# Performance work log

Hardware: AMD Instinct MI355X
Metric: run time of the kernel (lower is better)

Reference implementation:

```python
import jax, jax.numpy as jnp
import numpy as np

N_STATE = 1024
N_HEAD = 16
HEAD_DIM = N_STATE // N_HEAD
SEQLENS = [1024, 896, 768, 640, 512, 384, 896, 1024]  # sum = 6144
TOTAL = sum(SEQLENS)


def setup_inputs() -> dict:
    key = jax.random.key(0)
    ks = jax.random.split(key, 8)
    s = 0.02
    cu = jnp.asarray(np.concatenate([[0], np.cumsum(SEQLENS)]), dtype=jnp.int32)
    return {
        "x": jax.random.normal(ks[0], (TOTAL, N_STATE), jnp.float32),
        "cu_seqlens": cu,
        "Wq": jax.random.normal(ks[1], (N_STATE, N_STATE), jnp.float32) * s,
        "bq": jax.random.normal(ks[2], (N_STATE,), jnp.float32) * s,
        "Wk": jax.random.normal(ks[3], (N_STATE, N_STATE), jnp.float32) * s,
        "Wv": jax.random.normal(ks[4], (N_STATE, N_STATE), jnp.float32) * s,
        "bv": jax.random.normal(ks[5], (N_STATE,), jnp.float32) * s,
        "Wo": jax.random.normal(ks[6], (N_STATE, N_STATE), jnp.float32) * s,
        "bo": jax.random.normal(ks[7], (N_STATE,), jnp.float32) * s,
    }


def reference(x, cu_seqlens, Wq, bq, Wk, Wv, bv, Wo, bo):
    # cu_seqlens is a static (host) quantity in the original (used via .tolist())
    cu = np.asarray(jax.device_get(cu_seqlens))
    seqlens = cu[1:] - cu[:-1]
    B = len(seqlens)
    Lmax = int(seqlens.max())

    q = x @ Wq.T + bq              # [T, n_state]
    k = x @ Wk.T                   # key has no bias
    v = x @ Wv.T + bv

    # static pad/unpad index maps (honoring the ragged structure)
    ar = np.arange(Lmax)
    valid = ar[None, :] < seqlens[:, None]             # [B, Lmax]
    idx = np.where(valid, cu[:-1, None] + ar[None, :], 0)
    unpad_idx = np.nonzero(valid.reshape(-1))[0]       # flat positions of real tokens
    valid_j = jnp.asarray(valid)

    def pad(t):  # [T, n_state] -> [B, Lmax, H, D], zeros in padding
        p = jnp.where(valid_j[:, :, None], t[idx], 0.0)
        return p.reshape(B, Lmax, N_HEAD, HEAD_DIM)

    qp, kp, vp = pad(q), pad(k), pad(v)
    scale = HEAD_DIM ** -0.5
    # torch adds the bool mask (True->1.0) after masked_fill(mask==0, -max):
    # valid keys get +1.0 (softmax-invariant shift), invalid keys get -finfo.max
    big_neg = jnp.finfo(x.dtype).max
    add_mask = jnp.where(valid_j, 1.0, -big_neg)[:, None, None, :]  # [B,1,1,Lmax]

    scores = jnp.einsum("bqhd,bkhd->bhqk", qp, kp) * scale + add_mask
    weights = jax.nn.softmax(scores, axis=-1)
    ctx = jnp.einsum("bhqk,bkhd->bqhd", weights, vp)   # [B, Lmax, H, D]
    ctx_flat = ctx.reshape(B * Lmax, N_STATE)[unpad_idx]  # [T, n_state]
    return ctx_flat @ Wo.T + bo
```

## Files before the change

kernel.cpp:

```cpp
#include <hip/hip_runtime.h>

typedef unsigned short u16;
typedef unsigned int u32;
typedef __attribute__((ext_vector_type(8))) short bf16x8;
typedef __attribute__((ext_vector_type(4))) float f32x4;

#define MFMA_BF16(a, b, c) __builtin_amdgcn_mfma_f32_16x16x32_bf16((a), (b), (c), 0, 0, 0)

#define QSCALE 0.18033688011112042f

__device__ __forceinline__ u16 f2bf(float f) {
    union { float f; unsigned u; } v; v.f = f;
    return (u16)((v.u + 0x7FFFu + ((v.u >> 16) & 1u)) >> 16);
}

__device__ __forceinline__ u32 pkbf(float a, float b) {
    union { float f; unsigned u; } x, y; x.f = a; y.f = b;
    return ((x.u + 0x8000u) >> 16) | ((y.u + 0x8000u) & 0xFFFF0000u);
}

__device__ __forceinline__ void async16(const void* g, void* l) {
    __builtin_amdgcn_global_load_lds(
        (const __attribute__((address_space(1))) void*)g,
        (__attribute__((address_space(3))) void*)l, 16, 0, 0);
}

__global__ __launch_bounds__(256) void cvt_all(
    const float* __restrict__ x, const float* __restrict__ Wq, const float* __restrict__ Wk,
    const float* __restrict__ Wv, const float* __restrict__ Wo,
    u16* __restrict__ xb, u16* __restrict__ Wqb, u16* __restrict__ Wkb,
    u16* __restrict__ Wvb, u16* __restrict__ Wob) {
    int b = blockIdx.x;
    const float* src; u16* dst; int base;
    if (b < 6144)      { src = x;  dst = xb;  base = b; }
    else if (b < 7168) { src = Wq; dst = Wqb; base = b - 6144; }
    else if (b < 8192) { src = Wk; dst = Wkb; base = b - 7168; }
    else if (b < 9216) { src = Wv; dst = Wvb; base = b - 8192; }
    else               { src = Wo; dst = Wob; base = b - 9216; }
    int i = base * 256 + threadIdx.x;
    float4 v = ((const float4*)src)[i];
    unsigned long long pk = (unsigned long long)f2bf(v.x)
                          | ((unsigned long long)f2bf(v.y) << 16)
                          | ((unsigned long long)f2bf(v.z) << 32)
                          | ((unsigned long long)f2bf(v.w) << 48);
    *(unsigned long long*)(dst + (size_t)i * 4) = pk;
}

__global__ __launch_bounds__(256) void gemm_qkv(
    const u16* __restrict__ xb,
    const u16* __restrict__ Wqb, const u16* __restrict__ Wkb, const u16* __restrict__ Wvb,
    const float* __restrict__ bq, const float* __restrict__ bv,
    u16* __restrict__ qb, u16* __restrict__ kb, u16* __restrict__ vbT) {
    __shared__ __align__(16) u16 As[2][128 * 64];
    __shared__ __align__(16) u16 Bs[2][128 * 64];
    const int tid = threadIdx.x;

    const int fid = blockIdx.x;
    const int xcd = fid & 7;
    const int slot = fid >> 3;
    const int mloc = slot % 6;
    const int nidx = slot / 6;
    const int m0 = (xcd * 6 + mloc) << 7;
    const int buf = nidx >> 3;
    const int n0 = (nidx & 7) << 7;
    const u16* __restrict__ W = (buf == 0) ? Wqb : (buf == 1) ? Wkb : Wvb;

    const int rr = tid >> 3;
    const int cg = tid & 7;
    const int wv = tid >> 6, lane = tid & 63, g = lane >> 4, c = lane & 15;
    const int wm = (wv & 1) << 6, wn = (wv >> 1) << 6;

    const int sw = (cg ^ (rr & 7)) << 3;
    const u16* gA[4]; const u16* gB[4];
#pragma unroll
    for (int r = 0; r < 4; ++r) {
        gA[r] = xb + (size_t)(m0 + (r << 5) + rr) * 1024 + sw;
        gB[r] = W + (size_t)(n0 + (r << 5) + rr) * 1024 + sw;
    }

    f32x4 zero = {0.f, 0.f, 0.f, 0.f};
    f32x4 acc[4][4];
#pragma unroll
    for (int i = 0; i < 4; ++i)
#pragma unroll
        for (int j = 0; j < 4; ++j) acc[i][j] = zero;

#pragma unroll
    for (int r = 0; r < 4; ++r) {
        async16(gA[r], &As[0][(r << 11) + tid * 8]);
        async16(gB[r], &Bs[0][(r << 11) + tid * 8]);
    }
#pragma unroll
    for (int r = 0; r < 4; ++r) {
        async16(gA[r] + 64, &As[1][(r << 11) + tid * 8]);
        async16(gB[r] + 64, &Bs[1][(r << 11) + tid * 8]);
    }
    asm volatile("s_waitcnt vmcnt(8)" ::: "memory");
    __builtin_amdgcn_s_barrier();
    __builtin_amdgcn_sched_barrier(0);

    for (int kt = 0; kt < 16; ++kt) {
        const int cur = kt & 1;
#pragma unroll
        for (int ks = 0; ks < 2; ++ks) {
            bf16x8 af[4], bb[4];
#pragma unroll
            for (int i = 0; i < 4; ++i) {
                int ra = wm + (i << 4) + c;
                af[i] = *(const bf16x8*)(&As[cur][ra * 64 + ((((ks << 2) + g) ^ (ra & 7)) << 3)]);
                int rb = wn + (i << 4) + c;
                bb[i] = *(const bf16x8*)(&Bs[cur][rb * 64 + ((((ks << 2) + g) ^ (rb & 7)) << 3)]);
            }
#pragma unroll
            for (int i = 0; i < 4; ++i)
#pragma unroll
                for (int j = 0; j < 4; ++j) acc[i][j] = MFMA_BF16(af[i], bb[j], acc[i][j]);
        }
        if (kt == 15) break;
        __builtin_amdgcn_sched_barrier(0);
        __builtin_amdgcn_s_barrier();
        if (kt < 14) {
            const int k0 = (kt + 2) << 6;
#pragma unroll
            for (int r = 0; r < 4; ++r) {
                async16(gA[r] + k0, &As[cur][(r << 11) + tid * 8]);
                async16(gB[r] + k0, &Bs[cur][(r << 11) + tid * 8]);
            }
            asm volatile("s_waitcnt vmcnt(8)" ::: "memory");
        } else {
            asm volatile("s_waitcnt vmcnt(0)" ::: "memory");
        }
        __builtin_amdgcn_s_barrier();
        __builtin_amdgcn_sched_barrier(0);
    }

    if (buf == 0) {
#pragma unroll
        for (int j = 0; j < 4; ++j) {
            int col = n0 + wn + (j << 4) + c;
            float bias = bq[col];
#pragma unroll
            for (int i = 0; i < 4; ++i) {
                int rowb = m0 + wm + (i << 4) + (g << 2);
#pragma unroll
                for (int r = 0; r < 4; ++r)
                    qb[(size_t)(rowb + r) * 1024 + col] = f2bf((acc[i][j][r] + bias) * QSCALE);
            }
        }
    } else if (buf == 1) {
#pragma unroll
        for (int j = 0; j < 4; ++j) {
            int col = n0 + wn + (j << 4) + c;
#pragma unroll
            for (int i = 0; i < 4; ++i) {
                int rowb = m0 + wm + (i << 4) + (g << 2);
#pragma unroll
                for (int r = 0; r < 4; ++r)
                    kb[(size_t)(rowb + r) * 1024 + col] = f2bf(acc[i][j][r]);
            }
        }
    } else {
#pragma unroll
        for (int j = 0; j < 4; ++j) {
            int col = n0 + wn + (j << 4) + c;
            float bias = bv[col];
#pragma unroll
            for (int i = 0; i < 4; ++i) {
                int trow = m0 + wm + (i << 4) + (g << 2);
                unsigned long long pk =
                      (unsigned long long)f2bf(acc[i][j][0] + bias)
                    | ((unsigned long long)f2bf(acc[i][j][1] + bias) << 16)
                    | ((unsigned long long)f2bf(acc[i][j][2] + bias) << 32)
                    | ((unsigned long long)f2bf(acc[i][j][3] + bias) << 48);
                *(unsigned long long*)(vbT + (size_t)col * 6144 + trow) = pk;
            }
        }
    }
}

__global__ __launch_bounds__(256) void gemm_out(
    const u16* __restrict__ ctxb, const u16* __restrict__ Wob,
    const float* __restrict__ bo, float* __restrict__ out) {
    __shared__ __align__(16) u16 As[2][64 * 64];
    __shared__ __align__(16) u16 Bs[2][64 * 64];
    const int tid = threadIdx.x;

    const int fid = blockIdx.x;
    const int xcd = fid & 7;
    const int slot = fid >> 3;
    const int mloc = slot % 12;
    const int nidx = slot / 12;
    const int m0 = (xcd * 12 + mloc) << 6;
    const int n0 = nidx << 6;

    const int rr = tid >> 3, cg = tid & 7;
    const int wv = tid >> 6, lane = tid & 63, g = lane >> 4, c = lane & 15;
    const int wm = (wv & 1) << 5, wn = (wv >> 1) << 5;

    const int sw = (cg ^ (rr & 7)) << 3;
    const u16* gA[2]; const u16* gB[2];
#pragma unroll
    for (int r = 0; r < 2; ++r) {
        gA[r] = ctxb + (size_t)(m0 + (r << 5) + rr) * 1024 + sw;
        gB[r] = Wob + (size_t)(n0 + (r << 5) + rr) * 1024 + sw;
    }

    f32x4 zero = {0.f, 0.f, 0.f, 0.f};
    f32x4 acc[2][2];
#pragma unroll
    for (int i = 0; i < 2; ++i)
#pragma unroll
        for (int j = 0; j < 2; ++j) acc[i][j] = zero;

#pragma unroll
    for (int r = 0; r < 2; ++r) {
        async16(gA[r], &As[0][(r << 11) + tid * 8]);
        async16(gB[r], &Bs[0][(r << 11) + tid * 8]);
    }
#pragma unroll
    for (int r = 0; r < 2; ++r) {
        async16(gA[r] + 64, &As[1][(r << 11) + tid * 8]);
        async16(gB[r] + 64, &Bs[1][(r << 11) + tid * 8]);
    }
    asm volatile("s_waitcnt vmcnt(4)" ::: "memory");
    __builtin_amdgcn_s_barrier();
    __builtin_amdgcn_sched_barrier(0);

    for (int kt = 0; kt < 16; ++kt) {
        const int cur = kt & 1;
#pragma unroll
        for (int ks = 0; ks < 2; ++ks) {
            bf16x8 af[2], bb[2];
#pragma unroll
            for (int i = 0; i < 2; ++i) {
                int ra = wm + (i << 4) + c;
                af[i] = *(const bf16x8*)(&As[cur][ra * 64 + ((((ks << 2) + g) ^ (ra & 7)) << 3)]);
                int rb = wn + (i << 4) + c;
                bb[i] = *(const bf16x8*)(&Bs[cur][rb * 64 + ((((ks << 2) + g) ^ (rb & 7)) << 3)]);
            }
#pragma unroll
            for (int i = 0; i < 2; ++i)
#pragma unroll
                for (int j = 0; j < 2; ++j) acc[i][j] = MFMA_BF16(af[i], bb[j], acc[i][j]);
        }
        if (kt == 15) break;
        __builtin_amdgcn_sched_barrier(0);
        __builtin_amdgcn_s_barrier();
        if (kt < 14) {
            const int k0 = (kt + 2) << 6;
#pragma unroll
            for (int r = 0; r < 2; ++r) {
                async16(gA[r] + k0, &As[cur][(r << 11) + tid * 8]);
                async16(gB[r] + k0, &Bs[cur][(r << 11) + tid * 8]);
            }
            asm volatile("s_waitcnt vmcnt(4)" ::: "memory");
        } else {
            asm volatile("s_waitcnt vmcnt(0)" ::: "memory");
        }
        __builtin_amdgcn_s_barrier();
        __builtin_amdgcn_sched_barrier(0);
    }

#pragma unroll
    for (int j = 0; j < 2; ++j) {
        int col = n0 + wn + (j << 4) + c;
        float bias = bo[col];
#pragma unroll
        for (int i = 0; i < 2; ++i) {
            int rowb = m0 + wm + (i << 4) + (g << 2);
#pragma unroll
            for (int r = 0; r < 4; ++r)
                out[(size_t)(rowb + r) * 1024 + col] = acc[i][j][r] + bias;
        }
    }
}

__global__ __launch_bounds__(256) void attn_kernel(const u16* __restrict__ qb,
                                                   const u16* __restrict__ kb,
                                                   const u16* __restrict__ vbT,
                                                   u16* __restrict__ ctxb) {
    __shared__ __align__(16) u16 Ks[128 * 64];
    __shared__ __align__(16) u16 Vs[64 * 128];
    __shared__ __align__(16) u16 Ps[4 * 2048];

    const int tid = threadIdx.x;
    const int fid = blockIdx.x;
    const int xcd = fid & 7;
    const int slot = fid >> 3;
    const int h = (xcd << 1) + (slot >= 96 ? 1 : 0);
    const int q0 = (slot % 96) << 6;

    const int cuv[9] = {0, 1024, 1920, 2688, 3328, 3840, 4224, 5120, 6144};
    int s0 = 0, e0 = 6144;
#pragma unroll
    for (int i = 1; i < 8; ++i) {
        if (q0 >= cuv[i]) s0 = cuv[i];
        if (q0 < cuv[i] && cuv[i] < e0) e0 = cuv[i];
    }
    const int ntiles = (e0 - s0) >> 7;

    const int wv = tid >> 6, lane = tid & 63, g = lane >> 4, c = lane & 15;
    const int wrow = wv << 4;

    {
        const int rr = tid >> 3, cg = tid & 7;
#pragma unroll
        for (int r = 0; r < 2; ++r) {
            int row = (r << 5) + rr;
            async16(qb + (size_t)(q0 + row) * 1024 + (h << 6) + ((cg ^ (row & 7)) << 3),
                    Ps + (r << 11) + tid * 8);
        }
    }
    __syncthreads();

    bf16x8 qf[2];
#pragma unroll
    for (int ks = 0; ks < 2; ++ks) {
        int row = wrow + c;
        qf[ks] = *(const bf16x8*)(Ps + row * 64 + ((((ks << 2) + g) ^ (row & 7)) << 3));
    }

    float m_run = -1e30f, l_run = 0.f;
    f32x4 zero = {0.f, 0.f, 0.f, 0.f};
    f32x4 oacc[4];
#pragma unroll
    for (int nt = 0; nt < 4; ++nt) oacc[nt] = zero;

    const int pbase = (wv << 11) + c * 128;
    const int c7 = c & 7;

    for (int kt = 0; kt < ntiles; ++kt) {
        const int kv0 = s0 + (kt << 7);
        __syncthreads();
        {
            const int rr = tid >> 3, cg = tid & 7;
#pragma unroll
            for (int r = 0; r < 4; ++r) {
                int row = (r << 5) + rr;
                async16(kb + (size_t)(kv0 + row) * 1024 + (h << 6) + ((cg ^ (row & 7)) << 3),
                        Ks + (r << 11) + tid * 8);
            }
            const int rr2 = tid >> 4, cg2 = tid & 15;
#pragma unroll
            for (int r = 0; r < 4; ++r) {
                int row = (r << 4) + rr2;
                async16(vbT + (size_t)((h << 6) + row) * 6144 + kv0 + ((cg2 ^ (row & 15)) << 3),
                        Vs + (r << 11) + tid * 8);
            }
        }
        __syncthreads();

        f32x4 st[8];
#pragma unroll
        for (int mt = 0; mt < 8; ++mt) st[mt] = zero;
#pragma unroll
        for (int mt = 0; mt < 8; ++mt) {
            int row = (mt << 4) + c;
            int sw = row & 7;
#pragma unroll
            for (int ks = 0; ks < 2; ++ks) {
                bf16x8 kf = *(const bf16x8*)(&Ks[row * 64 + ((((ks << 2) + g) ^ sw) << 3)]);
                st[mt] = MFMA_BF16(kf, qf[ks], st[mt]);
            }
        }

        float mx = st[0][0];
#pragma unroll
        for (int mt = 0; mt < 8; ++mt)
#pragma unroll
            for (int r = 0; r < 4; ++r) mx = fmaxf(mx, st[mt][r]);
        mx = fmaxf(mx, __shfl_xor(mx, 16, 64));
        mx = fmaxf(mx, __shfl_xor(mx, 32, 64));
        float mnew = fmaxf(m_run, mx);
        float alpha = exp2f(m_run - mnew);
        m_run = mnew;

        float rsum = 0.f;
#pragma unroll
        for (int mt = 0; mt < 8; ++mt) {
            float p0 = exp2f(st[mt][0] - mnew);
            float p1 = exp2f(st[mt][1] - mnew);
            float p2 = exp2f(st[mt][2] - mnew);
            float p3 = exp2f(st[mt][3] - mnew);
            rsum += (p0 + p1) + (p2 + p3);
            int ph = ((mt << 2) + g) ^ (c7 << 1);
            *(uint2*)(Ps + pbase + (ph << 2)) = make_uint2(pkbf(p0, p1), pkbf(p2, p3));
        }
        rsum += __shfl_xor(rsum, 16, 64);
        rsum += __shfl_xor(rsum, 32, 64);
        l_run = l_run * alpha + rsum;

        float al[4];
#pragma unroll
        for (int r = 0; r < 4; ++r) al[r] = __shfl(alpha, (g << 2) + r, 16);
#pragma unroll
        for (int nt = 0; nt < 4; ++nt)
#pragma unroll
            for (int r = 0; r < 4; ++r) oacc[nt][r] *= al[r];

#pragma unroll
        for (int ks = 0; ks < 4; ++ks) {
            int pg = ((ks << 2) + g) ^ c7;
            bf16x8 pf = *(const bf16x8*)(Ps + pbase + (pg << 3));
#pragma unroll
            for (int nt = 0; nt < 4; ++nt) {
                int vrow = (nt << 4) + c;
                bf16x8 vf = *(const bf16x8*)(&Vs[vrow * 128 + ((((ks << 2) + g) ^ (vrow & 15)) << 3)]);
                oacc[nt] = MFMA_BF16(pf, vf, oacc[nt]);
            }
        }
    }

    float inv = 1.0f / l_run;
    float invr[4];
#pragma unroll
    for (int r = 0; r < 4; ++r) invr[r] = __shfl(inv, (g << 2) + r, 16);
#pragma unroll
    for (int r = 0; r < 4; ++r) {
        size_t rowoff = (size_t)(q0 + wrow + (g << 2) + r) * 1024 + (h << 6);
#pragma unroll
        for (int nt = 0; nt < 4; ++nt)
            ctxb[rowoff + (nt << 4) + c] = f2bf(oacc[nt][r] * invr[r]);
    }
}

extern "C" void kernel_launch(void* const* d_in, const int* in_sizes, int n_in,
                              void* d_out, int out_size, void* d_ws, size_t ws_size,
                              hipStream_t stream) {
    const float* x  = (const float*)d_in[0];
    const float* Wq = (const float*)d_in[2];
    const float* bq = (const float*)d_in[3];
    const float* Wk = (const float*)d_in[4];
    const float* Wv = (const float*)d_in[5];
    const float* bv = (const float*)d_in[6];
    const float* Wo = (const float*)d_in[7];
    const float* bo = (const float*)d_in[8];
    float* out = (float*)d_out;

    u16* ws = (u16*)d_ws;
    u16* xb   = ws;
    u16* Wqb  = xb + 6291456;
    u16* Wkb  = Wqb + 1048576;
    u16* Wvb  = Wkb + 1048576;
    u16* Wob  = Wvb + 1048576;
    u16* qb   = Wob + 1048576;
    u16* kb   = qb + 6291456;
    u16* vbT  = kb + 6291456;
    u16* ctxb = xb;

    cvt_all<<<10240, 256, 0, stream>>>(x, Wq, Wk, Wv, Wo, xb, Wqb, Wkb, Wvb, Wob);
    gemm_qkv<<<1152, 256, 0, stream>>>(xb, Wqb, Wkb, Wvb, bq, bv, qb, kb, vbT);
    attn_kernel<<<1536, 256, 0, stream>>>(qb, kb, vbT, ctxb);
    gemm_out<<<1536, 256, 0, stream>>>(ctxb, Wob, bo, out);
}
```

Measured before the change: 228.5 us.

## Load attention K/V/Q fragments directly from global memory and skip rescales

The attention kernel drops the shared-memory staging of Q, K and V tiles and the two block barriers per KV tile. Each wave now reads its MFMA operand fragments straight from global memory, relying on L2/cache reuse across the four waves, and launch bounds request 4 blocks per SM for occupancy. Online-softmax rescaling is skipped unless the new row max exceeds the running max by more than 8 in the log2 domain, which removes exp and multiply work on most tiles. In exchange, global loads are redundant across waves and less coalesced. Skipping the rescale lets probabilities reach up to 2^8 before the bf16 packing, which is a small numerical risk.

After: 332.5 us. 1.45x slower.

```diff
diff --git a/kernel.cpp b/kernel.cpp
--- a/kernel.cpp
+++ b/kernel.cpp
@@ -275,12 +275,10 @@
     }
 }
 
-__global__ __launch_bounds__(256) void attn_kernel(const u16* __restrict__ qb,
-                                                   const u16* __restrict__ kb,
-                                                   const u16* __restrict__ vbT,
-                                                   u16* __restrict__ ctxb) {
-    __shared__ __align__(16) u16 Ks[128 * 64];
-    __shared__ __align__(16) u16 Vs[64 * 128];
+__global__ __launch_bounds__(256, 4) void attn_kernel(const u16* __restrict__ qb,
+                                                      const u16* __restrict__ kb,
+                                                      const u16* __restrict__ vbT,
+                                                      u16* __restrict__ ctxb) {
     __shared__ __align__(16) u16 Ps[4 * 2048];
 
     const int tid = threadIdx.x;
@@ -302,23 +300,10 @@
     const int wv = tid >> 6, lane = tid & 63, g = lane >> 4, c = lane & 15;
     const int wrow = wv << 4;
 
-    {
-        const int rr = tid >> 3, cg = tid & 7;
-#pragma unroll
-        for (int r = 0; r < 2; ++r) {
-            int row = (r << 5) + rr;
-            async16(qb + (size_t)(q0 + row) * 1024 + (h << 6) + ((cg ^ (row & 7)) << 3),
-                    Ps + (r << 11) + tid * 8);
-        }
-    }
-    __syncthreads();
-
+    const u16* qp = qb + (size_t)(q0 + wrow + c) * 1024 + (h << 6) + (g << 3);
     bf16x8 qf[2];
-#pragma unroll
-    for (int ks = 0; ks < 2; ++ks) {
-        int row = wrow + c;
-        qf[ks] = *(const bf16x8*)(Ps + row * 64 + ((((ks << 2) + g) ^ (row & 7)) << 3));
-    }
+    qf[0] = *(const bf16x8*)(qp);
+    qf[1] = *(const bf16x8*)(qp + 32);
 
     float m_run = -1e30f, l_run = 0.f;
     f32x4 zero = {0.f, 0.f, 0.f, 0.f};
@@ -329,39 +314,23 @@
     const int pbase = (wv << 11) + c * 128;
     const int c7 = c & 7;
 
+    const u16* kbase0 = kb + (size_t)(s0 + c) * 1024 + (h << 6) + (g << 3);
+    const u16* vbase0 = vbT + (size_t)((h << 6) + c) * 6144 + s0 + (g << 3);
+
     for (int kt = 0; kt < ntiles; ++kt) {
-        const int kv0 = s0 + (kt << 7);
-        __syncthreads();
-        {
-            const int rr = tid >> 3, cg = tid & 7;
-#pragma unroll
-            for (int r = 0; r < 4; ++r) {
-                int row = (r << 5) + rr;
-                async16(kb + (size_t)(kv0 + row) * 1024 + (h << 6) + ((cg ^ (row & 7)) << 3),
-                        Ks + (r << 11) + tid * 8);
-            }
-            const int rr2 = tid >> 4, cg2 = tid & 15;
-#pragma unroll
-            for (int r = 0; r < 4; ++r) {
-                int row = (r << 4) + rr2;
-                async16(vbT + (size_t)((h << 6) + row) * 6144 + kv0 + ((cg2 ^ (row & 15)) << 3),
-                        Vs + (r << 11) + tid * 8);
-            }
-        }
-        __syncthreads();
+        const u16* kbase = kbase0 + (size_t)(kt << 7) * 1024;
+        const u16* vbase = vbase0 + (kt << 7);
 
         f32x4 st[8];
 #pragma unroll
         for (int mt = 0; mt < 8; ++mt) st[mt] = zero;
 #pragma unroll
         for (int mt = 0; mt < 8; ++mt) {
-            int row = (mt << 4) + c;
-            int sw = row & 7;
-#pragma unroll
-            for (int ks = 0; ks < 2; ++ks) {
-                bf16x8 kf = *(const bf16x8*)(&Ks[row * 64 + ((((ks << 2) + g) ^ sw) << 3)]);
-                st[mt] = MFMA_BF16(kf, qf[ks], st[mt]);
-            }
+            const u16* kr = kbase + (size_t)(mt << 4) * 1024;
+            bf16x8 kf0 = *(const bf16x8*)(kr);
+            bf16x8 kf1 = *(const bf16x8*)(kr + 32);
+            st[mt] = MFMA_BF16(kf0, qf[0], st[mt]);
+            st[mt] = MFMA_BF16(kf1, qf[1], st[mt]);
         }
 
         float mx = st[0][0];
@@ -371,32 +340,35 @@
             for (int r = 0; r < 4; ++r) mx = fmaxf(mx, st[mt][r]);
         mx = fmaxf(mx, __shfl_xor(mx, 16, 64));
         mx = fmaxf(mx, __shfl_xor(mx, 32, 64));
-        float mnew = fmaxf(m_run, mx);
-        float alpha = exp2f(m_run - mnew);
-        m_run = mnew;
+
+        if (!__all(mx - m_run <= 8.f)) {
+            float mnew = fmaxf(m_run, mx);
+            float alpha = exp2f(m_run - mnew);
+            m_run = mnew;
+            l_run *= alpha;
+            float al[4];
+#pragma unroll
+            for (int r = 0; r < 4; ++r) al[r] = __shfl(alpha, (g << 2) + r, 16);
+#pragma unroll
+            for (int nt = 0; nt < 4; ++nt)
+#pragma unroll
+                for (int r = 0; r < 4; ++r) oacc[nt][r] *= al[r];
+        }
 
         float rsum = 0.f;
 #pragma unroll
         for (int mt = 0; mt < 8; ++mt) {
-            float p0 = exp2f(st[mt][0] - mnew);
-            float p1 = exp2f(st[mt][1] - mnew);
-            float p2 = exp2f(st[mt][2] - mnew);
-            float p3 = exp2f(st[mt][3] - mnew);
+            float p0 = exp2f(st[mt][0] - m_run);
+            float p1 = exp2f(st[mt][1] - m_run);
+            float p2 = exp2f(st[mt][2] - m_run);
+            float p3 = exp2f(st[mt][3] - m_run);
             rsum += (p0 + p1) + (p2 + p3);
             int ph = ((mt << 2) + g) ^ (c7 << 1);
             *(uint2*)(Ps + pbase + (ph << 2)) = make_uint2(pkbf(p0, p1), pkbf(p2, p3));
         }
         rsum += __shfl_xor(rsum, 16, 64);
         rsum += __shfl_xor(rsum, 32, 64);
-        l_run = l_run * alpha + rsum;
-
-        float al[4];
-#pragma unroll
-        for (int r = 0; r < 4; ++r) al[r] = __shfl(alpha, (g << 2) + r, 16);
-#pragma unroll
-        for (int nt = 0; nt < 4; ++nt)
-#pragma unroll
-            for (int r = 0; r < 4; ++r) oacc[nt][r] *= al[r];
+        l_run += rsum;
 
 #pragma unroll
         for (int ks = 0; ks < 4; ++ks) {
@@ -404,8 +376,7 @@
             bf16x8 pf = *(const bf16x8*)(Ps + pbase + (pg << 3));
 #pragma unroll
             for (int nt = 0; nt < 4; ++nt) {
-                int vrow = (nt << 4) + c;
-                bf16x8 vf = *(const bf16x8*)(&Vs[vrow * 128 + ((((ks << 2) + g) ^ (vrow & 15)) << 3)]);
+                bf16x8 vf = *(const bf16x8*)(vbase + (size_t)(nt << 4) * 6144 + (ks << 5));
                 oacc[nt] = MFMA_BF16(pf, vf, oacc[nt]);
             }
         }
```

## Lazy softmax rescaling, MFMA row sums, hardware bf16 pack, direct Q loads

Applied to the files above, without the earlier changes.

Reworks the attention inner loop in several ways. The online-softmax rescale of the output and sum accumulators now runs only when the running max grows by more than a threshold anywhere in the wave. The row-sum shuffles are replaced by an extra MFMA against a vector of ones, and probabilities are packed with the hardware bf16 convert instruction. Q is loaded straight from global memory into registers instead of staging through LDS with a barrier, and MFMA sections get raised wave priority. The lazy rescale allows exponents up to 2^8 above the stored max, which may cost some precision, and the MFMA row sum adds matrix work on every tile.

Result: no change. 227.0 us (-0.7%).

```diff
diff --git a/kernel.cpp b/kernel.cpp
--- a/kernel.cpp
+++ b/kernel.cpp
@@ -14,9 +14,10 @@
     return (u16)((v.u + 0x7FFFu + ((v.u >> 16) & 1u)) >> 16);
 }
 
-__device__ __forceinline__ u32 pkbf(float a, float b) {
-    union { float f; unsigned u; } x, y; x.f = a; y.f = b;
-    return ((x.u + 0x8000u) >> 16) | ((y.u + 0x8000u) & 0xFFFF0000u);
+__device__ __forceinline__ u32 cvtpk(float a, float b) {
+    u32 r;
+    asm("v_cvt_pk_bf16_f32 %0, %1, %2" : "=v"(r) : "v"(a), "v"(b));
+    return r;
 }
 
 __device__ __forceinline__ void async16(const void* g, void* l) {
@@ -302,29 +303,20 @@
     const int wv = tid >> 6, lane = tid & 63, g = lane >> 4, c = lane & 15;
     const int wrow = wv << 4;
 
-    {
-        const int rr = tid >> 3, cg = tid & 7;
-#pragma unroll
-        for (int r = 0; r < 2; ++r) {
-            int row = (r << 5) + rr;
-            async16(qb + (size_t)(q0 + row) * 1024 + (h << 6) + ((cg ^ (row & 7)) << 3),
-                    Ps + (r << 11) + tid * 8);
-        }
-    }
-    __syncthreads();
-
-    bf16x8 qf[2];
-#pragma unroll
-    for (int ks = 0; ks < 2; ++ks) {
-        int row = wrow + c;
-        qf[ks] = *(const bf16x8*)(Ps + row * 64 + ((((ks << 2) + g) ^ (row & 7)) << 3));
-    }
-
-    float m_run = -1e30f, l_run = 0.f;
+    const u16* qp = qb + (size_t)(q0 + wrow + c) * 1024 + (h << 6) + (g << 3);
+    bf16x8 qf0 = *(const bf16x8*)(qp);
+    bf16x8 qf1 = *(const bf16x8*)(qp + 32);
+
+    float m_run = -1e30f;
     f32x4 zero = {0.f, 0.f, 0.f, 0.f};
     f32x4 oacc[4];
 #pragma unroll
     for (int nt = 0; nt < 4; ++nt) oacc[nt] = zero;
+    f32x4 lacc = zero;
+
+    const short one_bf = (short)0x3F80;
+    const bf16x8 vones = {one_bf, one_bf, one_bf, one_bf,
+                          one_bf, one_bf, one_bf, one_bf};
 
     const int pbase = (wv << 11) + c * 128;
     const int c7 = c & 7;
@@ -353,55 +345,58 @@
         f32x4 st[8];
 #pragma unroll
         for (int mt = 0; mt < 8; ++mt) st[mt] = zero;
+        __builtin_amdgcn_s_setprio(1);
 #pragma unroll
         for (int mt = 0; mt < 8; ++mt) {
             int row = (mt << 4) + c;
             int sw = row & 7;
-#pragma unroll
-            for (int ks = 0; ks < 2; ++ks) {
-                bf16x8 kf = *(const bf16x8*)(&Ks[row * 64 + ((((ks << 2) + g) ^ sw) << 3)]);
-                st[mt] = MFMA_BF16(kf, qf[ks], st[mt]);
-            }
-        }
-
-        float mx = st[0][0];
-#pragma unroll
-        for (int mt = 0; mt < 8; ++mt)
-#pragma unroll
-            for (int r = 0; r < 4; ++r) mx = fmaxf(mx, st[mt][r]);
+            bf16x8 kf0 = *(const bf16x8*)(&Ks[row * 64 + ((g ^ sw) << 3)]);
+            bf16x8 kf1 = *(const bf16x8*)(&Ks[row * 64 + (((4 + g) ^ sw) << 3)]);
+            st[mt] = MFMA_BF16(kf0, qf0, st[mt]);
+            st[mt] = MFMA_BF16(kf1, qf1, st[mt]);
+        }
+        __builtin_amdgcn_s_setprio(0);
+
+        float mx = fmaxf(fmaxf(st[0][0], st[0][1]), fmaxf(st[0][2], st[0][3]));
+#pragma unroll
+        for (int mt = 1; mt < 8; ++mt) {
+            float a = fmaxf(st[mt][0], fmaxf(st[mt][1], st[mt][2]));
+            mx = fmaxf(mx, fmaxf(a, st[mt][3]));
+        }
         mx = fmaxf(mx, __shfl_xor(mx, 16, 64));
         mx = fmaxf(mx, __shfl_xor(mx, 32, 64));
-        float mnew = fmaxf(m_run, mx);
-        float alpha = exp2f(m_run - mnew);
-        m_run = mnew;
-
-        float rsum = 0.f;
+
+        if (!__all(mx - m_run <= 8.f)) {
+            float mnew = fmaxf(m_run, mx);
+            float alpha = exp2f(m_run - mnew);
+            m_run = mnew;
+            float al[4];
+#pragma unroll
+            for (int r = 0; r < 4; ++r) al[r] = __shfl(alpha, (g << 2) + r, 16);
+#pragma unroll
+            for (int nt = 0; nt < 4; ++nt)
+#pragma unroll
+                for (int r = 0; r < 4; ++r) oacc[nt][r] *= al[r];
+#pragma unroll
+            for (int r = 0; r < 4; ++r) lacc[r] *= al[r];
+        }
+
 #pragma unroll
         for (int mt = 0; mt < 8; ++mt) {
-            float p0 = exp2f(st[mt][0] - mnew);
-            float p1 = exp2f(st[mt][1] - mnew);
-            float p2 = exp2f(st[mt][2] - mnew);
-            float p3 = exp2f(st[mt][3] - mnew);
-            rsum += (p0 + p1) + (p2 + p3);
+            float p0 = exp2f(st[mt][0] - m_run);
+            float p1 = exp2f(st[mt][1] - m_run);
+            float p2 = exp2f(st[mt][2] - m_run);
+            float p3 = exp2f(st[mt][3] - m_run);
             int ph = ((mt << 2) + g) ^ (c7 << 1);
-            *(uint2*)(Ps + pbase + (ph << 2)) = make_uint2(pkbf(p0, p1), pkbf(p2, p3));
-        }
-        rsum += __shfl_xor(rsum, 16, 64);
-        rsum += __shfl_xor(rsum, 32, 64);
-        l_run = l_run * alpha + rsum;
-
-        float al[4];
-#pragma unroll
-        for (int r = 0; r < 4; ++r) al[r] = __shfl(alpha, (g << 2) + r, 16);
-#pragma unroll
-        for (int nt = 0; nt < 4; ++nt)
-#pragma unroll
-            for (int r = 0; r < 4; ++r) oacc[nt][r] *= al[r];
-
+            *(uint2*)(Ps + pbase + (ph << 2)) = make_uint2(cvtpk(p0, p1), cvtpk(p2, p3));
+        }
+
+        __builtin_amdgcn_s_setprio(1);
 #pragma unroll
         for (int ks = 0; ks < 4; ++ks) {
             int pg = ((ks << 2) + g) ^ c7;
             bf16x8 pf = *(const bf16x8*)(Ps + pbase + (pg << 3));
+            lacc = MFMA_BF16(pf, vones, lacc);
 #pragma unroll
             for (int nt = 0; nt < 4; ++nt) {
                 int vrow = (nt << 4) + c;
@@ -409,12 +404,12 @@
                 oacc[nt] = MFMA_BF16(pf, vf, oacc[nt]);
             }
         }
-    }
-
-    float inv = 1.0f / l_run;
+        __builtin_amdgcn_s_setprio(0);
+    }
+
     float invr[4];
 #pragma unroll
-    for (int r = 0; r < 4; ++r) invr[r] = __shfl(inv, (g << 2) + r, 16);
+    for (int r = 0; r < 4; ++r) invr[r] = 1.0f / lacc[r];
 #pragma unroll
     for (int r = 0; r < 4; ++r) {
         size_t rowoff = (size_t)(q0 + wrow + (g << 2) + r) * 1024 + (h << 6);
```
